# Kernel optimization log

Hardware: AMD Instinct MI355X
Metric: run time of the kernel (lower is better)

## Reference

```python
import jax, jax.numpy as jnp
import numpy as np

N = 40000      # input points
M = 40000      # output points
E = 500000     # flat neighbor edges (ragged flattened)
F = 32         # input feature channels
C = 64         # output channels
K = 15         # kernel points
EXTENT = 0.6


def _make_kernel_points(k, radius):
    # Deterministic stand-in for load_kernels(): first point fixed at center,
    # remaining points spread inside a ball of the given radius.
    rng = np.random.RandomState(0)
    pts = rng.randn(k, 3).astype(np.float32)
    pts /= np.linalg.norm(pts, axis=1, keepdims=True) + 1e-9
    scale = rng.rand(k, 1).astype(np.float32) ** (1.0 / 3.0)
    pts = pts * scale * radius
    pts[0] = 0.0  # fixed='center'
    return jnp.asarray(pts)


def setup_inputs() -> dict:
    key = jax.random.key(0)
    ks = jax.random.split(key, 6)
    points = jax.random.uniform(ks[0], (N, 3), dtype=jnp.float32)
    features = jax.random.normal(ks[1], (N, F), dtype=jnp.float32)
    output_points = jax.random.uniform(ks[2], (M, 3), dtype=jnp.float32)
    neighbor_indices = jax.random.randint(ks[3], (E,), 0, N, dtype=jnp.int32)
    segment_ids = jnp.sort(jax.random.randint(ks[4], (E,), 0, M, dtype=jnp.int32))
    k_points = _make_kernel_points(K, 1.5 * EXTENT)          # [K,3] constant
    k_values = jax.random.normal(ks[5], (K, F, C), dtype=jnp.float32) * 0.05
    return {
        "points": points,
        "features": features,
        "output_points": output_points,
        "neighbor_indices": neighbor_indices,
        "segment_ids": segment_ids,
        "k_points": k_points,
        "k_values": k_values,
    }


def reference(points, features, output_points, neighbor_indices, segment_ids,
              k_points, k_values):
    # Gather neighbor coords/features and recenter around each output point.
    rel = points[neighbor_indices] - output_points[segment_ids]      # [E,3]
    nbr_feat = features[neighbor_indices]                            # [E,F]

    # Per-kernel-point squared distances and linear influence weights.
    diff = rel[:, None, :] - k_points[None, :, :]                    # [E,K,3]
    sq_dist = jnp.sum(diff * diff, axis=-1)                          # [E,K]
    w = jnp.maximum(1.0 - jnp.sqrt(sq_dist) / EXTENT, 0.0)           # [E,K]

    # Weighted features and ragged segment-sum per output point.
    weighted = w[:, :, None] * nbr_feat[:, None, :]                  # [E,K,F]
    agg = jax.ops.segment_sum(weighted, segment_ids, num_segments=M,
                              indices_are_sorted=True)               # [M,K,F]

    # Batched matmul over kernel points, then sum over kernel points.
    out = jnp.einsum('mkf,kfc->mc', agg, k_values)                   # [M,C]
    return out
```

## Files before the change

### kernel.cpp

```cpp
#include <hip/hip_runtime.h>

typedef __attribute__((ext_vector_type(8))) short bf16x8;
typedef __attribute__((ext_vector_type(4))) float f32x4;
typedef __attribute__((ext_vector_type(4))) _Float16 f16x4;

#define NPTS   40000
#define MOUT   40000
#define EDG    500000
#define FIN    32
#define COUT   64
#define KP     15
#define KFDIM  (KP * FIN)
#define TM     16
#define ASTRIDE 488
#define EXTENT 0.6f

__device__ __forceinline__ short f2bf(float x) {
    union { float f; unsigned u; } v; v.f = x;
    unsigned r = (v.u + 0x7fffu + ((v.u >> 16) & 1u)) >> 16;
    return (short)r;
}

__global__ __launch_bounds__(256) void feat_to_f16(
    const float* __restrict__ features, _Float16* __restrict__ feat_h)
{
    const int i = (blockIdx.x * 256 + threadIdx.x) * 4;
    const float4 v = *(const float4*)(features + i);
    feat_h[i + 0] = (_Float16)v.x;
    feat_h[i + 1] = (_Float16)v.y;
    feat_h[i + 2] = (_Float16)v.z;
    feat_h[i + 3] = (_Float16)v.w;
}

__global__ __launch_bounds__(256) void pts_to_f4(
    const float* __restrict__ pts, float4* __restrict__ p4)
{
    const int i = blockIdx.x * 256 + threadIdx.x;
    if (i < NPTS) {
        const float* p = pts + 3 * i;
        p4[i] = make_float4(p[0], p[1], p[2], 0.f);
    }
}

__global__ __launch_bounds__(256) void build_row_starts(
    const int* __restrict__ seg_ids, int* __restrict__ row_start)
{
    const int e = blockIdx.x * 256 + threadIdx.x;
    if (e >= EDG) return;
    const int cur  = seg_ids[e];
    const int prev = (e == 0) ? -1 : seg_ids[e - 1];
    for (int m = prev + 1; m <= cur; ++m) row_start[m] = e;
    if (e == EDG - 1)
        for (int m = cur + 1; m <= MOUT; ++m) row_start[m] = EDG;
}

__global__ __launch_bounds__(256, 8) void kpconv_agg_mfma16(
    const float4* __restrict__ points4,
    const _Float16* __restrict__ feat_h,
    const float* __restrict__ output_points,
    const int*   __restrict__ nbr_idx,
    const int*   __restrict__ row_start,
    const float* __restrict__ k_points,
    unsigned short* __restrict__ agg_g)
{
    const int tid  = threadIdx.x;
    const int wave = tid >> 6;
    const int lane = tid & 63;
    const int quad = lane >> 4;
    const int l16  = lane & 15;

    const int m = blockIdx.x * 4 + wave;
    const int e0 = row_start[m], e1 = row_start[m + 1];

    const float ox = output_points[m * 3 + 0];
    const float oy = output_points[m * 3 + 1];
    const float oz = output_points[m * 3 + 2];

    const int myk = l16 < KP ? l16 : 0;
    const float kpx = k_points[myk * 3 + 0];
    const float kpy = k_points[myk * 3 + 1];
    const float kpz = k_points[myk * 3 + 2];
    const float inv_ext = 1.f / EXTENT;

    f32x4 c_lo = {0.f, 0.f, 0.f, 0.f};
    f32x4 c_hi = {0.f, 0.f, 0.f, 0.f};

    for (int es = e0; es < e1; es += 16) {
        const int last = e1 - 1;
        const int ebase = es + quad * 4;

        int nb[4];
        #pragma unroll
        for (int j = 0; j < 4; ++j) {
            const int e = ebase + j;
            nb[j] = nbr_idx[e < e1 ? e : last];
        }

        f16x4 afrag, blo, bhi;
        #pragma unroll
        for (int j = 0; j < 4; ++j) {
            const float4 p = points4[nb[j]];
            const float rx = p.x - ox;
            const float ry = p.y - oy;
            const float rz = p.z - oz;
            const float dx = rx - kpx, dy = ry - kpy, dz = rz - kpz;
            const float d2 = dx * dx + dy * dy + dz * dz;
            float w = 1.f - sqrtf(d2) * inv_ext;
            w = w > 0.f ? w : 0.f;
            if (l16 >= KP || ebase + j >= e1) w = 0.f;
            afrag[j] = (_Float16)w;
        }

        #pragma unroll
        for (int j = 0; j < 4; ++j) {
            const _Float16* fp = feat_h + nb[j] * FIN + l16;
            blo[j] = fp[0];
            bhi[j] = fp[16];
        }

        c_lo = __builtin_amdgcn_mfma_f32_16x16x16f16(afrag, blo, c_lo, 0, 0, 0);
        c_hi = __builtin_amdgcn_mfma_f32_16x16x16f16(afrag, bhi, c_hi, 0, 0, 0);
    }

    unsigned short* dst = agg_g + (size_t)m * KFDIM;
    #pragma unroll
    for (int r = 0; r < 4; ++r) {
        const int krow = quad * 4 + r;
        if (krow < KP) {
            dst[krow * FIN + l16]      = (unsigned short)f2bf(c_lo[r]);
            dst[krow * FIN + 16 + l16] = (unsigned short)f2bf(c_hi[r]);
        }
    }
}

__global__ __launch_bounds__(256, 4) void kpconv_gemm(
    const unsigned short* __restrict__ agg_g,
    const float* __restrict__ k_values,
    float* __restrict__ out)
{
    const int tid  = threadIdx.x;
    const int wave = tid >> 6;
    const int lane = tid & 63;
    const int quad = lane >> 4;
    const int l16  = lane & 15;
    const int m0   = blockIdx.x * 32;
    const int bcol = wave * 16 + l16;

    bf16x8 bfr[15];
    #pragma unroll
    for (int s = 0; s < 15; ++s) {
        #pragma unroll
        for (int j = 0; j < 8; ++j)
            bfr[s][j] = f2bf(k_values[(32 * s + quad * 8 + j) * COUT + bcol]);
    }

    const unsigned short* arow0 = agg_g + (size_t)(m0 + l16) * KFDIM + quad * 8;
    const unsigned short* arow1 = arow0 + 16 * KFDIM;

    f32x4 c0 = {0.f, 0.f, 0.f, 0.f};
    f32x4 c1 = {0.f, 0.f, 0.f, 0.f};
    #pragma unroll
    for (int s = 0; s < 15; ++s) {
        const bf16x8 a0 = *(const bf16x8*)(arow0 + 32 * s);
        const bf16x8 a1 = *(const bf16x8*)(arow1 + 32 * s);
        c0 = __builtin_amdgcn_mfma_f32_16x16x32_bf16(a0, bfr[s], c0, 0, 0, 0);
        c1 = __builtin_amdgcn_mfma_f32_16x16x32_bf16(a1, bfr[s], c1, 0, 0, 0);
    }

    #pragma unroll
    for (int r = 0; r < 4; ++r) {
        out[(m0 + quad * 4 + r) * COUT + bcol]      = c0[r];
        out[(m0 + 16 + quad * 4 + r) * COUT + bcol] = c1[r];
    }
}

__global__ __launch_bounds__(256, 4) void kpconv_agg_mfma(
    const float* __restrict__ points,
    const float* __restrict__ features,
    const float* __restrict__ output_points,
    const int*   __restrict__ nbr_idx,
    const int*   __restrict__ seg_ids,
    const float* __restrict__ k_points,
    unsigned short* __restrict__ agg_g)
{
    __shared__ int seg_start[5];

    const int tid  = threadIdx.x;
    const int m0   = blockIdx.x * 4;

    if (tid <= 4) {
        const int target = m0 + tid;
        int lo = 0, hi = EDG;
        while (lo < hi) {
            int mid = (lo + hi) >> 1;
            if (seg_ids[mid] < target) lo = mid + 1; else hi = mid;
        }
        seg_start[tid] = lo;
    }
    __syncthreads();

    const int wave = tid >> 6;
    const int lane = tid & 63;
    const int quad = lane >> 4;
    const int l16  = lane & 15;

    const int m = m0 + wave;
    const float ox = output_points[m * 3 + 0];
    const float oy = output_points[m * 3 + 1];
    const float oz = output_points[m * 3 + 2];

    const int myk = l16 < KP ? l16 : 0;
    const float kpx = k_points[myk * 3 + 0];
    const float kpy = k_points[myk * 3 + 1];
    const float kpz = k_points[myk * 3 + 2];
    const float inv_ext = 1.f / EXTENT;

    const int e0 = seg_start[wave], e1 = seg_start[wave + 1];

    f32x4 c_lo = {0.f, 0.f, 0.f, 0.f};
    f32x4 c_hi = {0.f, 0.f, 0.f, 0.f};

    for (int es = e0; es < e1; es += 32) {
        const int last = e1 - 1;
        const int ebase = es + quad * 8;

        int nb[8];
        #pragma unroll
        for (int j = 0; j < 8; ++j) {
            const int e = ebase + j;
            nb[j] = nbr_idx[e < e1 ? e : last];
        }

        bf16x8 afrag, blo, bhi;
        #pragma unroll
        for (int j = 0; j < 8; ++j) {
            const float* pp = points + nb[j] * 3;
            const float rx = pp[0] - ox;
            const float ry = pp[1] - oy;
            const float rz = pp[2] - oz;
            const float dx = rx - kpx, dy = ry - kpy, dz = rz - kpz;
            const float d2 = dx * dx + dy * dy + dz * dz;
            float w = 1.f - sqrtf(d2) * inv_ext;
            w = w > 0.f ? w : 0.f;
            if (l16 >= KP || ebase + j >= e1) w = 0.f;
            afrag[j] = f2bf(w);
        }

        #pragma unroll
        for (int j = 0; j < 8; ++j) {
            const float* fp = features + nb[j] * FIN + l16;
            blo[j] = f2bf(fp[0]);
            bhi[j] = f2bf(fp[16]);
        }

        c_lo = __builtin_amdgcn_mfma_f32_16x16x32_bf16(afrag, blo, c_lo, 0, 0, 0);
        c_hi = __builtin_amdgcn_mfma_f32_16x16x32_bf16(afrag, bhi, c_hi, 0, 0, 0);
    }

    unsigned short* dst = agg_g + (size_t)m * KFDIM;
    #pragma unroll
    for (int r = 0; r < 4; ++r) {
        const int krow = quad * 4 + r;
        if (krow < KP) {
            dst[krow * FIN + l16]      = (unsigned short)f2bf(c_lo[r]);
            dst[krow * FIN + 16 + l16] = (unsigned short)f2bf(c_hi[r]);
        }
    }
}

extern "C" void kernel_launch(void* const* d_in, const int* in_sizes, int n_in,
                              void* d_out, int out_size, void* d_ws, size_t ws_size,
                              hipStream_t stream) {
    const float* points        = (const float*)d_in[0];
    const float* features      = (const float*)d_in[1];
    const float* output_points = (const float*)d_in[2];
    const int*   nbr_idx       = (const int*)d_in[3];
    const int*   seg_ids       = (const int*)d_in[4];
    const float* k_points      = (const float*)d_in[5];
    const float* k_values      = (const float*)d_in[6];
    float* out = (float*)d_out;

    const size_t feat_bytes = (size_t)NPTS * FIN * sizeof(_Float16);
    const size_t pts4_bytes = (size_t)NPTS * sizeof(float4);
    const size_t rs_bytes   = ((size_t)(MOUT + 1) * sizeof(int) + 15) & ~15ul;
    const size_t agg_bytes  = (size_t)MOUT * KFDIM * sizeof(unsigned short);
    const size_t full_bytes = feat_bytes + pts4_bytes + rs_bytes + agg_bytes;

    if (ws_size >= full_bytes) {
        char* p = (char*)d_ws;
        _Float16* feat_h      = (_Float16*)p;            p += feat_bytes;
        float4*   points4     = (float4*)p;              p += pts4_bytes;
        int*      row_start   = (int*)p;                 p += rs_bytes;
        unsigned short* agg_g = (unsigned short*)p;

        feat_to_f16<<<NPTS * FIN / 1024, 256, 0, stream>>>(features, feat_h);
        pts_to_f4<<<(NPTS + 255) / 256, 256, 0, stream>>>(points, points4);
        build_row_starts<<<(EDG + 255) / 256, 256, 0, stream>>>(seg_ids, row_start);
        kpconv_agg_mfma16<<<MOUT / 4, 256, 0, stream>>>(
            points4, feat_h, output_points, nbr_idx, row_start, k_points, agg_g);
        kpconv_gemm<<<MOUT / 32, 256, 0, stream>>>(agg_g, k_values, out);
    } else {
        unsigned short* agg_g = (unsigned short*)d_ws;
        kpconv_agg_mfma<<<MOUT / 4, 256, 0, stream>>>(
            points, features, output_points, nbr_idx, seg_ids, k_points, agg_g);
        kpconv_gemm<<<MOUT / 32, 256, 0, stream>>>(agg_g, k_values, out);
    }
}
```

Before: 126.8 us.

## Fuse aggregation with GEMM via LDS and merge preprocessing kernels

Merges the three preprocessing kernels into one launch that branches on block index. Fuses the per-output-point MFMA aggregation with the kernel-weight GEMM: each block aggregates 16 output points into shared memory as bf16, then does the 16x64 GEMM from LDS. This removes the global agg buffer round trip (about 38MB written then read) and two launches. In exchange each block loads and converts all k_values into registers, and each wave now handles four output points in sequence, which cuts the number of waves in flight.

```diff
diff --git a/kernel.cpp b/kernel.cpp
--- a/kernel.cpp
+++ b/kernel.cpp
@@ -11,9 +11,13 @@
 #define COUT   64
 #define KP     15
 #define KFDIM  (KP * FIN)
-#define TM     16
 #define ASTRIDE 488
 #define EXTENT 0.6f
+
+#define FEAT_BLKS  (NPTS * FIN / 1024)
+#define PTS_BLKS   ((NPTS + 255) / 256)
+#define ROW_BLKS   ((EDG + 255) / 256)
+#define PRE_BLKS   (FEAT_BLKS + PTS_BLKS + ROW_BLKS)
 
 __device__ __forceinline__ short f2bf(float x) {
     union { float f; unsigned u; } v; v.f = x;
@@ -21,60 +25,63 @@
     return (short)r;
 }
 
-__global__ __launch_bounds__(256) void feat_to_f16(
-    const float* __restrict__ features, _Float16* __restrict__ feat_h)
-{
-    const int i = (blockIdx.x * 256 + threadIdx.x) * 4;
-    const float4 v = *(const float4*)(features + i);
-    feat_h[i + 0] = (_Float16)v.x;
-    feat_h[i + 1] = (_Float16)v.y;
-    feat_h[i + 2] = (_Float16)v.z;
-    feat_h[i + 3] = (_Float16)v.w;
-}
-
-__global__ __launch_bounds__(256) void pts_to_f4(
-    const float* __restrict__ pts, float4* __restrict__ p4)
-{
-    const int i = blockIdx.x * 256 + threadIdx.x;
-    if (i < NPTS) {
-        const float* p = pts + 3 * i;
-        p4[i] = make_float4(p[0], p[1], p[2], 0.f);
-    }
-}
-
-__global__ __launch_bounds__(256) void build_row_starts(
+__global__ __launch_bounds__(256) void preprocess_all(
+    const float* __restrict__ features, _Float16* __restrict__ feat_h,
+    const float* __restrict__ pts, float4* __restrict__ p4,
     const int* __restrict__ seg_ids, int* __restrict__ row_start)
 {
-    const int e = blockIdx.x * 256 + threadIdx.x;
-    if (e >= EDG) return;
-    const int cur  = seg_ids[e];
-    const int prev = (e == 0) ? -1 : seg_ids[e - 1];
-    for (int m = prev + 1; m <= cur; ++m) row_start[m] = e;
-    if (e == EDG - 1)
-        for (int m = cur + 1; m <= MOUT; ++m) row_start[m] = EDG;
-}
-
-__global__ __launch_bounds__(256, 8) void kpconv_agg_mfma16(
+    const int bid = blockIdx.x;
+    if (bid < FEAT_BLKS) {
+        const int i = (bid * 256 + threadIdx.x) * 4;
+        const float4 v = *(const float4*)(features + i);
+        feat_h[i + 0] = (_Float16)v.x;
+        feat_h[i + 1] = (_Float16)v.y;
+        feat_h[i + 2] = (_Float16)v.z;
+        feat_h[i + 3] = (_Float16)v.w;
+    } else if (bid < FEAT_BLKS + PTS_BLKS) {
+        const int i = (bid - FEAT_BLKS) * 256 + threadIdx.x;
+        if (i < NPTS) {
+            const float* p = pts + 3 * i;
+            p4[i] = make_float4(p[0], p[1], p[2], 0.f);
+        }
+    } else {
+        const int e = (bid - FEAT_BLKS - PTS_BLKS) * 256 + threadIdx.x;
+        if (e >= EDG) return;
+        const int cur  = seg_ids[e];
+        const int prev = (e == 0) ? -1 : seg_ids[e - 1];
+        for (int m = prev + 1; m <= cur; ++m) row_start[m] = e;
+        if (e == EDG - 1)
+            for (int m = cur + 1; m <= MOUT; ++m) row_start[m] = EDG;
+    }
+}
+
+__global__ __launch_bounds__(256, 4) void kpconv_fused_mfma(
     const float4* __restrict__ points4,
     const _Float16* __restrict__ feat_h,
     const float* __restrict__ output_points,
     const int*   __restrict__ nbr_idx,
     const int*   __restrict__ row_start,
     const float* __restrict__ k_points,
-    unsigned short* __restrict__ agg_g)
+    const float* __restrict__ k_values,
+    float* __restrict__ out)
 {
+    __shared__ __align__(16) unsigned short agg[16 * ASTRIDE];
+
     const int tid  = threadIdx.x;
     const int wave = tid >> 6;
     const int lane = tid & 63;
     const int quad = lane >> 4;
     const int l16  = lane & 15;
-
-    const int m = blockIdx.x * 4 + wave;
-    const int e0 = row_start[m], e1 = row_start[m + 1];
-
-    const float ox = output_points[m * 3 + 0];
-    const float oy = output_points[m * 3 + 1];
-    const float oz = output_points[m * 3 + 2];
+    const int m0   = blockIdx.x * 16;
+
+    bf16x8 bfr[15];
+    const int bcol = wave * 16 + l16;
+    #pragma unroll
+    for (int s = 0; s < 15; ++s) {
+        #pragma unroll
+        for (int j = 0; j < 8; ++j)
+            bfr[s][j] = f2bf(k_values[(32 * s + quad * 8 + j) * COUT + bcol]);
+    }
 
     const int myk = l16 < KP ? l16 : 0;
     const float kpx = k_points[myk * 3 + 0];
@@ -82,44 +89,163 @@
     const float kpz = k_points[myk * 3 + 2];
     const float inv_ext = 1.f / EXTENT;
 
+    for (int s = 0; s < 4; ++s) {
+        const int li = wave * 4 + s;
+        const int m  = m0 + li;
+        const int e0 = row_start[m], e1 = row_start[m + 1];
+
+        const float ox = output_points[m * 3 + 0];
+        const float oy = output_points[m * 3 + 1];
+        const float oz = output_points[m * 3 + 2];
+
+        f32x4 c_lo = {0.f, 0.f, 0.f, 0.f};
+        f32x4 c_hi = {0.f, 0.f, 0.f, 0.f};
+
+        for (int es = e0; es < e1; es += 16) {
+            const int last = e1 - 1;
+            const int ebase = es + quad * 4;
+
+            int nb[4];
+            #pragma unroll
+            for (int j = 0; j < 4; ++j) {
+                const int e = ebase + j;
+                nb[j] = nbr_idx[e < e1 ? e : last];
+            }
+
+            f16x4 afrag, blo, bhi;
+            #pragma unroll
+            for (int j = 0; j < 4; ++j) {
+                const float4 p = points4[nb[j]];
+                const float rx = p.x - ox;
+                const float ry = p.y - oy;
+                const float rz = p.z - oz;
+                const float dx = rx - kpx, dy = ry - kpy, dz = rz - kpz;
+                const float d2 = dx * dx + dy * dy + dz * dz;
+                float w = 1.f - sqrtf(d2) * inv_ext;
+                w = w > 0.f ? w : 0.f;
+                if (l16 >= KP || ebase + j >= e1) w = 0.f;
+                afrag[j] = (_Float16)w;
+            }
+
+            #pragma unroll
+            for (int j = 0; j < 4; ++j) {
+                const _Float16* fp = feat_h + nb[j] * FIN + l16;
+                blo[j] = fp[0];
+                bhi[j] = fp[16];
+            }
+
+            c_lo = __builtin_amdgcn_mfma_f32_16x16x16f16(afrag, blo, c_lo, 0, 0, 0);
+            c_hi = __builtin_amdgcn_mfma_f32_16x16x16f16(afrag, bhi, c_hi, 0, 0, 0);
+        }
+
+        unsigned short* dst = agg + li * ASTRIDE;
+        #pragma unroll
+        for (int r = 0; r < 4; ++r) {
+            const int krow = quad * 4 + r;
+            if (krow < KP) {
+                dst[krow * FIN + l16]      = (unsigned short)f2bf(c_lo[r]);
+                dst[krow * FIN + 16 + l16] = (unsigned short)f2bf(c_hi[r]);
+            }
+        }
+    }
+
+    __syncthreads();
+
+    f32x4 c = {0.f, 0.f, 0.f, 0.f};
+    #pragma unroll
+    for (int s = 0; s < 15; ++s) {
+        const bf16x8 af = *(const bf16x8*)&agg[l16 * ASTRIDE + 32 * s + quad * 8];
+        c = __builtin_amdgcn_mfma_f32_16x16x32_bf16(af, bfr[s], c, 0, 0, 0);
+    }
+
+    #pragma unroll
+    for (int r = 0; r < 4; ++r) {
+        const int row = quad * 4 + r;
+        out[(m0 + row) * COUT + bcol] = c[r];
+    }
+}
+
+__global__ __launch_bounds__(256, 4) void kpconv_agg_mfma(
+    const float* __restrict__ points,
+    const float* __restrict__ features,
+    const float* __restrict__ output_points,
+    const int*   __restrict__ nbr_idx,
+    const int*   __restrict__ seg_ids,
+    const float* __restrict__ k_points,
+    unsigned short* __restrict__ agg_g)
+{
+    __shared__ int seg_start[5];
+
+    const int tid  = threadIdx.x;
+    const int m0   = blockIdx.x * 4;
+
+    if (tid <= 4) {
+        const int target = m0 + tid;
+        int lo = 0, hi = EDG;
+        while (lo < hi) {
+            int mid = (lo + hi) >> 1;
+            if (seg_ids[mid] < target) lo = mid + 1; else hi = mid;
+        }
+        seg_start[tid] = lo;
+    }
+    __syncthreads();
+
+    const int wave = tid >> 6;
+    const int lane = tid & 63;
+    const int quad = lane >> 4;
+    const int l16  = lane & 15;
+
+    const int m = m0 + wave;
+    const float ox = output_points[m * 3 + 0];
+    const float oy = output_points[m * 3 + 1];
+    const float oz = output_points[m * 3 + 2];
+
+    const int myk = l16 < KP ? l16 : 0;
+    const float kpx = k_points[myk * 3 + 0];
+    const float kpy = k_points[myk * 3 + 1];
+    const float kpz = k_points[myk * 3 + 2];
+    const float inv_ext = 1.f / EXTENT;
+
+    const int e0 = seg_start[wave], e1 = seg_start[wave + 1];
+
     f32x4 c_lo = {0.f, 0.f, 0.f, 0.f};
     f32x4 c_hi = {0.f, 0.f, 0.f, 0.f};
 
-    for (int es = e0; es < e1; es += 16) {
+    for (int es = e0; es < e1; es += 32) {
         const int last = e1 - 1;
-        const int ebase = es + quad * 4;
-
-        int nb[4];
-        #pragma unroll
-        for (int j = 0; j < 4; ++j) {
+        const int ebase = es + quad * 8;
+
+        int nb[8];
+        #pragma unroll
+        for (int j = 0; j < 8; ++j) {
             const int e = ebase + j;
             nb[j] = nbr_idx[e < e1 ? e : last];
         }
 
-        f16x4 afrag, blo, bhi;
-        #pragma unroll
-        for (int j = 0; j < 4; ++j) {
-            const float4 p = points4[nb[j]];
-            const float rx = p.x - ox;
-            const float ry = p.y - oy;
-            const float rz = p.z - oz;
+        bf16x8 afrag, blo, bhi;
+        #pragma unroll
+        for (int j = 0; j < 8; ++j) {
+            const float* pp = points + nb[j] * 3;
+            const float rx = pp[0] - ox;
+            const float ry = pp[1] - oy;
+            const float rz = pp[2] - oz;
             const float dx = rx - kpx, dy = ry - kpy, dz = rz - kpz;
             const float d2 = dx * dx + dy * dy + dz * dz;
             float w = 1.f - sqrtf(d2) * inv_ext;
             w = w > 0.f ? w : 0.f;
             if (l16 >= KP || ebase + j >= e1) w = 0.f;
-            afrag[j] = (_Float16)w;
-        }
-
-        #pragma unroll
-        for (int j = 0; j < 4; ++j) {
-            const _Float16* fp = feat_h + nb[j] * FIN + l16;
-            blo[j] = fp[0];
-            bhi[j] = fp[16];
-        }
-
-        c_lo = __builtin_amdgcn_mfma_f32_16x16x16f16(afrag, blo, c_lo, 0, 0, 0);
-        c_hi = __builtin_amdgcn_mfma_f32_16x16x16f16(afrag, bhi, c_hi, 0, 0, 0);
+            afrag[j] = f2bf(w);
+        }
+
+        #pragma unroll
+        for (int j = 0; j < 8; ++j) {
+            const float* fp = features + nb[j] * FIN + l16;
+            blo[j] = f2bf(fp[0]);
+            bhi[j] = f2bf(fp[16]);
+        }
+
+        c_lo = __builtin_amdgcn_mfma_f32_16x16x32_bf16(afrag, blo, c_lo, 0, 0, 0);
+        c_hi = __builtin_amdgcn_mfma_f32_16x16x32_bf16(afrag, bhi, c_hi, 0, 0, 0);
     }
 
     unsigned short* dst = agg_g + (size_t)m * KFDIM;
@@ -174,100 +300,6 @@
     }
 }
 
-__global__ __launch_bounds__(256, 4) void kpconv_agg_mfma(
-    const float* __restrict__ points,
-    const float* __restrict__ features,
-    const float* __restrict__ output_points,
-    const int*   __restrict__ nbr_idx,
-    const int*   __restrict__ seg_ids,
-    const float* __restrict__ k_points,
-    unsigned short* __restrict__ agg_g)
-{
-    __shared__ int seg_start[5];
-
-    const int tid  = threadIdx.x;
-    const int m0   = blockIdx.x * 4;
-
-    if (tid <= 4) {
-        const int target = m0 + tid;
-        int lo = 0, hi = EDG;
-        while (lo < hi) {
-            int mid = (lo + hi) >> 1;
-            if (seg_ids[mid] < target) lo = mid + 1; else hi = mid;
-        }
-        seg_start[tid] = lo;
-    }
-    __syncthreads();
-
-    const int wave = tid >> 6;
-    const int lane = tid & 63;
-    const int quad = lane >> 4;
-    const int l16  = lane & 15;
-
-    const int m = m0 + wave;
-    const float ox = output_points[m * 3 + 0];
-    const float oy = output_points[m * 3 + 1];
-    const float oz = output_points[m * 3 + 2];
-
-    const int myk = l16 < KP ? l16 : 0;
-    const float kpx = k_points[myk * 3 + 0];
-    const float kpy = k_points[myk * 3 + 1];
-    const float kpz = k_points[myk * 3 + 2];
-    const float inv_ext = 1.f / EXTENT;
-
-    const int e0 = seg_start[wave], e1 = seg_start[wave + 1];
-
-    f32x4 c_lo = {0.f, 0.f, 0.f, 0.f};
-    f32x4 c_hi = {0.f, 0.f, 0.f, 0.f};
-
-    for (int es = e0; es < e1; es += 32) {
-        const int last = e1 - 1;
-        const int ebase = es + quad * 8;
-
-        int nb[8];
-        #pragma unroll
-        for (int j = 0; j < 8; ++j) {
-            const int e = ebase + j;
-            nb[j] = nbr_idx[e < e1 ? e : last];
-        }
-
-        bf16x8 afrag, blo, bhi;
-        #pragma unroll
-        for (int j = 0; j < 8; ++j) {
-            const float* pp = points + nb[j] * 3;
-            const float rx = pp[0] - ox;
-            const float ry = pp[1] - oy;
-            const float rz = pp[2] - oz;
-            const float dx = rx - kpx, dy = ry - kpy, dz = rz - kpz;
-            const float d2 = dx * dx + dy * dy + dz * dz;
-            float w = 1.f - sqrtf(d2) * inv_ext;
-            w = w > 0.f ? w : 0.f;
-            if (l16 >= KP || ebase + j >= e1) w = 0.f;
-            afrag[j] = f2bf(w);
-        }
-
-        #pragma unroll
-        for (int j = 0; j < 8; ++j) {
-            const float* fp = features + nb[j] * FIN + l16;
-            blo[j] = f2bf(fp[0]);
-            bhi[j] = f2bf(fp[16]);
-        }
-
-        c_lo = __builtin_amdgcn_mfma_f32_16x16x32_bf16(afrag, blo, c_lo, 0, 0, 0);
-        c_hi = __builtin_amdgcn_mfma_f32_16x16x32_bf16(afrag, bhi, c_hi, 0, 0, 0);
-    }
-
-    unsigned short* dst = agg_g + (size_t)m * KFDIM;
-    #pragma unroll
-    for (int r = 0; r < 4; ++r) {
-        const int krow = quad * 4 + r;
-        if (krow < KP) {
-            dst[krow * FIN + l16]      = (unsigned short)f2bf(c_lo[r]);
-            dst[krow * FIN + 16 + l16] = (unsigned short)f2bf(c_hi[r]);
-        }
-    }
-}
-
 extern "C" void kernel_launch(void* const* d_in, const int* in_sizes, int n_in,
                               void* d_out, int out_size, void* d_ws, size_t ws_size,
                               hipStream_t stream) {
@@ -283,22 +315,19 @@
     const size_t feat_bytes = (size_t)NPTS * FIN * sizeof(_Float16);
     const size_t pts4_bytes = (size_t)NPTS * sizeof(float4);
     const size_t rs_bytes   = ((size_t)(MOUT + 1) * sizeof(int) + 15) & ~15ul;
-    const size_t agg_bytes  = (size_t)MOUT * KFDIM * sizeof(unsigned short);
-    const size_t full_bytes = feat_bytes + pts4_bytes + rs_bytes + agg_bytes;
+    const size_t full_bytes = feat_bytes + pts4_bytes + rs_bytes;
 
     if (ws_size >= full_bytes) {
         char* p = (char*)d_ws;
-        _Float16* feat_h      = (_Float16*)p;            p += feat_bytes;
-        float4*   points4     = (float4*)p;              p += pts4_bytes;
-        int*      row_start   = (int*)p;                 p += rs_bytes;
-        unsigned short* agg_g = (unsigned short*)p;
-
-        feat_to_f16<<<NPTS * FIN / 1024, 256, 0, stream>>>(features, feat_h);
-        pts_to_f4<<<(NPTS + 255) / 256, 256, 0, stream>>>(points, points4);
-        build_row_starts<<<(EDG + 255) / 256, 256, 0, stream>>>(seg_ids, row_start);
-        kpconv_agg_mfma16<<<MOUT / 4, 256, 0, stream>>>(
-            points4, feat_h, output_points, nbr_idx, row_start, k_points, agg_g);
-        kpconv_gemm<<<MOUT / 32, 256, 0, stream>>>(agg_g, k_values, out);
+        _Float16* feat_h    = (_Float16*)p;  p += feat_bytes;
+        float4*   points4   = (float4*)p;    p += pts4_bytes;
+        int*      row_start = (int*)p;
+
+        preprocess_all<<<PRE_BLKS, 256, 0, stream>>>(
+            features, feat_h, points, points4, seg_ids, row_start);
+        kpconv_fused_mfma<<<MOUT / 16, 256, 0, stream>>>(
+            points4, feat_h, output_points, nbr_idx, row_start,
+            k_points, k_values, out);
     } else {
         unsigned short* agg_g = (unsigned short*)d_ws;
         kpconv_agg_mfma<<<MOUT / 4, 256, 0, stream>>>(
```

After: 187.0 us. 47.5% more time.
